# Optimization experiments

Measured on AMD Instinct MI355X. Metric: run time of the kernel, lower is better.

The kernel has to match this reference:

```python
import jax, jax.numpy as jnp
import numpy as np

HID = 256

def _linear(x, W, b):
    # torch nn.Linear: x @ W.T + b
    return x @ W.T + b

def setup_inputs() -> dict:
    key = jax.random.key(0)
    ks = jax.random.split(key, 9)
    N = 8192
    s = 1.0 / np.sqrt(HID)
    inp = {
        'query': jax.random.normal(ks[0], (N, HID), dtype=jnp.float32),
        'key':   jax.random.normal(ks[1], (N, HID), dtype=jnp.float32),
        'value': jax.random.normal(ks[2], (N, HID), dtype=jnp.float32),
        'Wq': jax.random.uniform(ks[3], (HID, HID), jnp.float32, -s, s),
        'bq': jax.random.uniform(ks[4], (HID,), jnp.float32, -s, s),
        'Wk': jax.random.uniform(ks[5], (HID, HID), jnp.float32, -s, s),
        'bk': jax.random.uniform(ks[6], (HID,), jnp.float32, -s, s),
        'Wv': jax.random.uniform(ks[7], (HID, HID), jnp.float32, -s, s),
        'bv': jax.random.uniform(ks[8], (HID,), jnp.float32, -s, s),
    }
    return inp

def reference(query, key, value, Wq, bq, Wk, bk, Wv, bv):
    q = _linear(query, Wq, bq)            # [N, H]
    k = _linear(key, Wk, bk)              # [N, H]
    v = _linear(value, Wv, bv)            # [N, H]
    q = q.reshape(-1, HID)
    k = k.reshape(-1, HID)
    v = v.reshape(-1, HID)
    attn = jax.nn.sigmoid(q @ k.T)        # [N, N], sigmoid attention (no softmax)
    return attn @ v                       # [N, H]
```

## Files before the change

### kernel.cpp

```cpp
#include <hip/hip_runtime.h>
#include <hip/hip_bf16.h>
#include <stdint.h>

#define HID 256
#define NTOK 8192

typedef unsigned short u16;
typedef unsigned int u32;

typedef __bf16 bf16x8 __attribute__((ext_vector_type(8)));
typedef float f32x4 __attribute__((ext_vector_type(4)));

__device__ __forceinline__ u16 f2bf(float f) {
  u32 u = __float_as_uint(f);
  u32 r = (u + 0x7FFFu + ((u >> 16) & 1u)) >> 16;
  return (u16)r;
}

__device__ __forceinline__ int swz(int row, int col, int ld) {
  return row * ld + ((((col >> 3) ^ (row & 7)) << 3) | (col & 7));
}

__global__ __launch_bounds__(256, 2) void proj_kernel(
    const float* __restrict__ Xq, const float* __restrict__ Xk, const float* __restrict__ Xv,
    const float* __restrict__ Wq, const float* __restrict__ Bq,
    const float* __restrict__ Wk, const float* __restrict__ Bk,
    const float* __restrict__ Wv, const float* __restrict__ Bv,
    u16* __restrict__ oq, u16* __restrict__ ok, u16* __restrict__ ovt)
{
  __shared__ __attribute__((aligned(16))) u16 Xs[64 * 64];
  __shared__ __attribute__((aligned(16))) u16 Ws[256 * 64];
  __shared__ __attribute__((aligned(16))) u16 Ts[64 * 256];

  const int tid = threadIdx.x;
  const int bid = blockIdx.x;
  const int sel = bid >> 7;
  const int m0 = (bid & 127) << 6;

  const float* X = sel == 0 ? Xq : (sel == 1 ? Xk : Xv);
  const float* W = sel == 0 ? Wq : (sel == 1 ? Wk : Wv);
  const float* B = sel == 0 ? Bq : (sel == 1 ? Bk : Bv);

  const int wid = tid >> 6;
  const int lane = tid & 63;
  const int ln = lane & 15;
  const int hi = lane >> 4;
  const int trow = tid >> 2;
  const int tq = tid & 3;

  f32x4 acc[4][4];
#pragma unroll
  for (int i = 0; i < 4; ++i)
#pragma unroll
    for (int j = 0; j < 4; ++j) acc[i][j] = (f32x4)0.f;

  for (int kc = 0; kc < 4; ++kc) {
    const int k0 = kc << 6;
    {
      const float* g = X + (size_t)(m0 + trow) * HID + k0 + tq * 16;
      u16 tmp[16];
#pragma unroll
      for (int e = 0; e < 16; e += 4) {
        float4 v = *reinterpret_cast<const float4*>(g + e);
        tmp[e] = f2bf(v.x); tmp[e + 1] = f2bf(v.y);
        tmp[e + 2] = f2bf(v.z); tmp[e + 3] = f2bf(v.w);
      }
      *reinterpret_cast<uint4*>(&Xs[swz(trow, tq * 16, 64)]) = *reinterpret_cast<uint4*>(&tmp[0]);
      *reinterpret_cast<uint4*>(&Xs[swz(trow, tq * 16 + 8, 64)]) = *reinterpret_cast<uint4*>(&tmp[8]);
    }
#pragma unroll
    for (int p = 0; p < 4; ++p) {
      int n = p * 64 + trow;
      const float* g = W + (size_t)n * HID + k0 + tq * 16;
      u16 tmp[16];
#pragma unroll
      for (int e = 0; e < 16; e += 4) {
        float4 v = *reinterpret_cast<const float4*>(g + e);
        tmp[e] = f2bf(v.x); tmp[e + 1] = f2bf(v.y);
        tmp[e + 2] = f2bf(v.z); tmp[e + 3] = f2bf(v.w);
      }
      *reinterpret_cast<uint4*>(&Ws[swz(n, tq * 16, 64)]) = *reinterpret_cast<uint4*>(&tmp[0]);
      *reinterpret_cast<uint4*>(&Ws[swz(n, tq * 16 + 8, 64)]) = *reinterpret_cast<uint4*>(&tmp[8]);
    }
    __syncthreads();
#pragma unroll
    for (int kk = 0; kk < 64; kk += 32) {
      bf16x8 a[4], b[4];
#pragma unroll
      for (int i = 0; i < 4; ++i)
        a[i] = *reinterpret_cast<bf16x8*>(&Xs[swz(i * 16 + ln, kk + hi * 8, 64)]);
#pragma unroll
      for (int j = 0; j < 4; ++j)
        b[j] = *reinterpret_cast<bf16x8*>(&Ws[swz(wid * 64 + j * 16 + ln, kk + hi * 8, 64)]);
#pragma unroll
      for (int i = 0; i < 4; ++i)
#pragma unroll
        for (int j = 0; j < 4; ++j)
          acc[i][j] = __builtin_amdgcn_mfma_f32_16x16x32_bf16(a[i], b[j], acc[i][j], 0, 0, 0);
    }
    __syncthreads();
  }

#pragma unroll
  for (int j = 0; j < 4; ++j) {
    int col = wid * 64 + j * 16 + ln;
    float bv = B[col];
#pragma unroll
    for (int i = 0; i < 4; ++i)
#pragma unroll
      for (int r = 0; r < 4; ++r) {
        int row = i * 16 + hi * 4 + r;
        Ts[row * HID + col] = f2bf(acc[i][j][r] + bv);
      }
  }
  __syncthreads();

  if (sel < 2) {
    u16* o = sel == 0 ? oq : ok;
#pragma unroll
    for (int i = 0; i < 8; ++i) {
      int slot = i * 256 + tid;
      int row = slot >> 5, s = slot & 31;
      uint4 v = *reinterpret_cast<uint4*>(&Ts[row * HID + s * 8]);
      *reinterpret_cast<uint4*>(&o[(size_t)(m0 + row) * HID + s * 8]) = v;
    }
  } else {
#pragma unroll
    for (int p = 0; p < 4; ++p) {
      int n = p * 64 + trow;
      int mseg = tq * 16;
      u16 tmp[16];
#pragma unroll
      for (int j2 = 0; j2 < 16; ++j2)
        tmp[j2] = Ts[(mseg + j2) * HID + n];
      *reinterpret_cast<uint4*>(&ovt[(size_t)n * NTOK + m0 + mseg]) = *reinterpret_cast<uint4*>(&tmp[0]);
      *reinterpret_cast<uint4*>(&ovt[(size_t)n * NTOK + m0 + mseg + 8]) = *reinterpret_cast<uint4*>(&tmp[8]);
    }
  }
}

#define QB 128
#define KVB 64
#define NSLICE 4
#define SLICE_LEN (NTOK / NSLICE)
#define NCH (SLICE_LEN / KVB)

__global__ __launch_bounds__(512, 2) void attn_kernel(
    const u16* __restrict__ qw, const u16* __restrict__ kw,
    const u16* __restrict__ vtw, float* __restrict__ out)
{
  __shared__ __attribute__((aligned(16))) u16 Qs[QB * HID];
  __shared__ __attribute__((aligned(16))) u16 Ks[KVB * HID];
  __shared__ __attribute__((aligned(16))) u16 Vs[HID * KVB];
  __shared__ __attribute__((aligned(16))) u16 Ps[QB * KVB];

  const int tid = threadIdx.x;
  const int bid = blockIdx.x;
  const int qt = bid >> 2, slice = bid & 3;
  const int m0 = qt * QB;
  const int kvbase = slice * SLICE_LEN;

  const int wid = tid >> 6, lane = tid & 63;
  const int ln = lane & 15, hi = lane >> 4;
  const int wr = wid >> 1, wc = wid & 1;

  auto stageQ = [&]() {
    int r_in = lane >> 5, s = lane & 31;
    for (int i = wid; i < 64; i += 8) {
      int r = i * 2 + r_in;
      const u16* g = qw + (size_t)(m0 + r) * HID + ((s ^ (r & 7)) << 3);
      __builtin_amdgcn_global_load_lds((const __attribute__((address_space(1))) u32*)g,
                                       (__attribute__((address_space(3))) u32*)(&Qs[i * 512]),
                                       16, 0, 0);
    }
  };
  auto stageK = [&](int ch) {
    int j0 = kvbase + ch * KVB;
    int r_in = lane >> 5, s = lane & 31;
    for (int i = wid; i < 32; i += 8) {
      int r = i * 2 + r_in;
      const u16* g = kw + (size_t)(j0 + r) * HID + ((s ^ (r & 7)) << 3);
      __builtin_amdgcn_global_load_lds((const __attribute__((address_space(1))) u32*)g,
                                       (__attribute__((address_space(3))) u32*)(&Ks[i * 512]),
                                       16, 0, 0);
    }
  };
  auto stageV = [&](int ch) {
    int j0 = kvbase + ch * KVB;
    int r_in = lane >> 3, s = lane & 7;
    for (int i = wid; i < 32; i += 8) {
      int d = i * 8 + r_in;
      const u16* g = vtw + (size_t)d * NTOK + j0 + ((s ^ (d & 7)) << 3);
      __builtin_amdgcn_global_load_lds((const __attribute__((address_space(1))) u32*)g,
                                       (__attribute__((address_space(3))) u32*)(&Vs[i * 512]),
                                       16, 0, 0);
    }
  };

  stageQ();
  stageK(0);
  stageV(0);

  f32x4 oacc[2][8];
#pragma unroll
  for (int i = 0; i < 2; ++i)
#pragma unroll
    for (int cb = 0; cb < 8; ++cb) oacc[i][cb] = (f32x4)0.f;

  __syncthreads();

  for (int c = 0; c < NCH; ++c) {
    f32x4 sacc[2][2];
#pragma unroll
    for (int i = 0; i < 2; ++i)
#pragma unroll
      for (int j = 0; j < 2; ++j) sacc[i][j] = (f32x4)0.f;

#pragma unroll
    for (int kk = 0; kk < 8; ++kk) {
      bf16x8 aq[2], bk[2];
#pragma unroll
      for (int i = 0; i < 2; ++i) {
        int qr = wr * 32 + i * 16 + ln;
        aq[i] = *reinterpret_cast<bf16x8*>(&Qs[qr * HID + ((((kk * 4 + hi) ^ (qr & 7))) << 3)]);
      }
#pragma unroll
      for (int j = 0; j < 2; ++j) {
        int kr = wc * 32 + j * 16 + ln;
        bk[j] = *reinterpret_cast<bf16x8*>(&Ks[kr * HID + ((((kk * 4 + hi) ^ (kr & 7))) << 3)]);
      }
#pragma unroll
      for (int i = 0; i < 2; ++i)
#pragma unroll
        for (int j = 0; j < 2; ++j)
          sacc[i][j] = __builtin_amdgcn_mfma_f32_16x16x32_bf16(aq[i], bk[j], sacc[i][j], 0, 0, 0);
    }

#pragma unroll
    for (int i = 0; i < 2; ++i)
#pragma unroll
      for (int j = 0; j < 2; ++j)
#pragma unroll
        for (int r = 0; r < 4; ++r) {
          float s = sacc[i][j][r];
          float p = __builtin_amdgcn_rcpf(1.0f + __expf(-s));
          int prow = wr * 32 + i * 16 + hi * 4 + r;
          int pcol = wc * 32 + j * 16 + ln;
          Ps[swz(prow, pcol, KVB)] = f2bf(p);
        }

    __syncthreads();
    if (c + 1 < NCH) stageK(c + 1);

#pragma unroll
    for (int ks = 0; ks < 2; ++ks) {
      bf16x8 ap[2];
#pragma unroll
      for (int i = 0; i < 2; ++i) {
        int pr = wr * 32 + i * 16 + ln;
        ap[i] = *reinterpret_cast<bf16x8*>(&Ps[pr * KVB + ((((ks * 4 + hi) ^ (pr & 7))) << 3)]);
      }
#pragma unroll
      for (int cb = 0; cb < 8; ++cb) {
        int vr = wc * 128 + cb * 16 + ln;
        bf16x8 bv = *reinterpret_cast<bf16x8*>(&Vs[vr * KVB + ((((ks * 4 + hi) ^ (vr & 7))) << 3)]);
#pragma unroll
        for (int i = 0; i < 2; ++i)
          oacc[i][cb] = __builtin_amdgcn_mfma_f32_16x16x32_bf16(ap[i], bv, oacc[i][cb], 0, 0, 0);
      }
    }

    __syncthreads();
    if (c + 1 < NCH) stageV(c + 1);
  }

#pragma unroll
  for (int i = 0; i < 2; ++i)
#pragma unroll
    for (int cb = 0; cb < 8; ++cb)
#pragma unroll
      for (int r = 0; r < 4; ++r) {
        int row = m0 + wr * 32 + i * 16 + hi * 4 + r;
        int col = wc * 128 + cb * 16 + ln;
        atomicAdd(&out[(size_t)row * HID + col], oacc[i][cb][r]);
      }
}

extern "C" void kernel_launch(void* const* d_in, const int* in_sizes, int n_in,
                              void* d_out, int out_size, void* d_ws, size_t ws_size,
                              hipStream_t stream) {
  const float* query = (const float*)d_in[0];
  const float* key_  = (const float*)d_in[1];
  const float* value = (const float*)d_in[2];
  const float* Wq = (const float*)d_in[3];
  const float* bq = (const float*)d_in[4];
  const float* Wk = (const float*)d_in[5];
  const float* bk = (const float*)d_in[6];
  const float* Wv = (const float*)d_in[7];
  const float* bv = (const float*)d_in[8];
  float* out = (float*)d_out;

  u16* qws  = (u16*)d_ws;
  u16* kws  = qws + (size_t)NTOK * HID;
  u16* vtws = kws + (size_t)NTOK * HID;

  hipMemsetAsync(d_out, 0, (size_t)NTOK * HID * sizeof(float), stream);
  proj_kernel<<<384, 256, 0, stream>>>(query, key_, value, Wq, bq, Wk, bk, Wv, bv,
                                       qws, kws, vtws);
  attn_kernel<<<256, 512, 0, stream>>>(qws, kws, vtws, out);
}
```

Measured before the change: 205.9 us.

## Rewrite attention with register-resident Q, 32x32 MFMA, permlane P, split-K fp16 partials

Rewrites all kernels. The attention kernel now holds a 256-row Q tile in registers per block and uses 32x32x16 MFMAs. It double-buffers K/V chunks of 32 tokens and passes sigmoid probabilities between lanes with permlane32 swaps instead of going through LDS. The key range is split into 8 slices that write fp16 partials, and a separate reduce kernel sums them, replacing the memset and float atomics. Weight conversion is moved to its own prepass and the projection is retiled to 128 rows. The cost is extra kernel launches, partial-buffer traffic, and fp16 range/precision risk in the partial outputs.

```diff
diff --git a/kernel.cpp b/kernel.cpp
--- a/kernel.cpp
+++ b/kernel.cpp
@@ -4,286 +4,268 @@
 
 #define HID 256
 #define NTOK 8192
+#define NS 8
+#define SLICE (NTOK / NS)
+#define CHUNK 32
+#define NCH (SLICE / CHUNK)
 
 typedef unsigned short u16;
 typedef unsigned int u32;
-
 typedef __bf16 bf16x8 __attribute__((ext_vector_type(8)));
-typedef float f32x4 __attribute__((ext_vector_type(4)));
+typedef float f32x16 __attribute__((ext_vector_type(16)));
+typedef __fp16 h16x2 __attribute__((ext_vector_type(2)));
+
+#define TAU(r, h) (((r) & 3) + 8 * ((r) >> 2) + 4 * (h))
 
 __device__ __forceinline__ u16 f2bf(float f) {
   u32 u = __float_as_uint(f);
-  u32 r = (u + 0x7FFFu + ((u >> 16) & 1u)) >> 16;
-  return (u16)r;
-}
-
-__device__ __forceinline__ int swz(int row, int col, int ld) {
-  return row * ld + ((((col >> 3) ^ (row & 7)) << 3) | (col & 7));
+  return (u16)((u + 0x7FFFu + ((u >> 16) & 1u)) >> 16);
+}
+
+__device__ __forceinline__ u32 cvtpk_bf16(float a, float b) {
+  u32 r;
+  asm("v_cvt_pk_bf16_f32 %0, %1, %2" : "=v"(r) : "v"(a), "v"(b));
+  return r;
+}
+
+__global__ void wcvt_kernel(const float* __restrict__ Wq, const float* __restrict__ Wk,
+                            const float* __restrict__ Wv, u16* __restrict__ out) {
+  int idx = blockIdx.x * 256 + threadIdx.x;
+  int mat = idx >> 14;
+  int off = (idx & 16383) << 2;
+  const float* src = mat == 0 ? Wq : (mat == 1 ? Wk : Wv);
+  float4 v = *reinterpret_cast<const float4*>(src + off);
+  ushort4 o;
+  o.x = f2bf(v.x); o.y = f2bf(v.y); o.z = f2bf(v.z); o.w = f2bf(v.w);
+  *reinterpret_cast<ushort4*>(out + mat * 65536 + off) = o;
 }
 
 __global__ __launch_bounds__(256, 2) void proj_kernel(
     const float* __restrict__ Xq, const float* __restrict__ Xk, const float* __restrict__ Xv,
-    const float* __restrict__ Wq, const float* __restrict__ Bq,
-    const float* __restrict__ Wk, const float* __restrict__ Bk,
-    const float* __restrict__ Wv, const float* __restrict__ Bv,
+    const u16* __restrict__ wcvt,
+    const float* __restrict__ Bq, const float* __restrict__ Bk, const float* __restrict__ Bv,
     u16* __restrict__ oq, u16* __restrict__ ok, u16* __restrict__ ovt)
 {
-  __shared__ __attribute__((aligned(16))) u16 Xs[64 * 64];
-  __shared__ __attribute__((aligned(16))) u16 Ws[256 * 64];
-  __shared__ __attribute__((aligned(16))) u16 Ts[64 * 256];
-
-  const int tid = threadIdx.x;
-  const int bid = blockIdx.x;
-  const int sel = bid >> 7;
-  const int m0 = (bid & 127) << 6;
+  __shared__ __attribute__((aligned(16))) unsigned char smem[32768 + 4 * 4352];
+  u16* wbuf0 = (u16*)smem;
+  u16* wbuf1 = (u16*)(smem + 16384);
+  float* scratch = (float*)(smem + 32768 + (threadIdx.x >> 6) * 4352);
+
+  const int tid = threadIdx.x, bid = blockIdx.x;
+  const int sel = bid >> 6;
+  const int m0 = (bid & 63) << 7;
+  const int wid = tid >> 6, l = tid & 63;
+  const int l31 = l & 31, lh = l >> 5;
 
   const float* X = sel == 0 ? Xq : (sel == 1 ? Xk : Xv);
-  const float* W = sel == 0 ? Wq : (sel == 1 ? Wk : Wv);
+  const u16* W = wcvt + sel * 65536;
   const float* B = sel == 0 ? Bq : (sel == 1 ? Bk : Bv);
-
-  const int wid = tid >> 6;
-  const int lane = tid & 63;
-  const int ln = lane & 15;
-  const int hi = lane >> 4;
-  const int trow = tid >> 2;
-  const int tq = tid & 3;
-
-  f32x4 acc[4][4];
-#pragma unroll
-  for (int i = 0; i < 4; ++i)
-#pragma unroll
-    for (int j = 0; j < 4; ++j) acc[i][j] = (f32x4)0.f;
-
-  for (int kc = 0; kc < 4; ++kc) {
-    const int k0 = kc << 6;
-    {
-      const float* g = X + (size_t)(m0 + trow) * HID + k0 + tq * 16;
+  const int mrow = m0 + wid * 32 + l31;
+
+  f32x16 acc[8];
+#pragma unroll
+  for (int nt = 0; nt < 8; ++nt) acc[nt] = (f32x16)0.f;
+
+  auto stageW = [&](int kc, u16* buf) {
+#pragma unroll
+    for (int ii = 0; ii < 4; ++ii) {
+      int u = (wid * 4 + ii) * 64 + l;
+      int ol = u >> 8, n = u & 255;
+      const u16* g = W + n * HID + kc * 32 + ol * 8;
+      __builtin_amdgcn_global_load_lds((const __attribute__((address_space(1))) u32*)g,
+                                       (__attribute__((address_space(3))) u32*)(buf + (size_t)u * 8),
+                                       16, 0, 0);
+    }
+  };
+
+  stageW(0, wbuf0);
+  __syncthreads();
+  for (int kc = 0; kc < 8; ++kc) {
+    u16* cur = (kc & 1) ? wbuf1 : wbuf0;
+    if (kc < 7) stageW(kc + 1, (kc & 1) ? wbuf0 : wbuf1);
+#pragma unroll
+    for (int k2 = 0; k2 < 2; ++k2) {
+      int ks = kc * 2 + k2;
+      float4 a0 = *reinterpret_cast<const float4*>(X + (size_t)mrow * HID + ks * 16 + lh * 8);
+      float4 a1 = *reinterpret_cast<const float4*>(X + (size_t)mrow * HID + ks * 16 + lh * 8 + 4);
+      union { u16 u[8]; bf16x8 v; } au;
+      au.u[0] = f2bf(a0.x); au.u[1] = f2bf(a0.y); au.u[2] = f2bf(a0.z); au.u[3] = f2bf(a0.w);
+      au.u[4] = f2bf(a1.x); au.u[5] = f2bf(a1.y); au.u[6] = f2bf(a1.z); au.u[7] = f2bf(a1.w);
+#pragma unroll
+      for (int nt = 0; nt < 8; ++nt) {
+        int unit = (k2 * 2 + lh) * 256 + nt * 32 + l31;
+        bf16x8 b = *reinterpret_cast<bf16x8*>(cur + (size_t)unit * 8);
+        acc[nt] = __builtin_amdgcn_mfma_f32_32x32x16_bf16(au.v, b, acc[nt], 0, 0, 0);
+      }
+    }
+    __syncthreads();
+  }
+
+#pragma unroll
+  for (int nt = 0; nt < 8; ++nt) {
+    float bv = B[nt * 32 + l31];
+#pragma unroll
+    for (int r = 0; r < 16; ++r)
+      scratch[TAU(r, lh) * 33 + l31] = acc[nt][r] + bv;
+    if (sel < 2) {
+      u16* o = sel == 0 ? oq : ok;
       u16 tmp[16];
 #pragma unroll
-      for (int e = 0; e < 16; e += 4) {
-        float4 v = *reinterpret_cast<const float4*>(g + e);
-        tmp[e] = f2bf(v.x); tmp[e + 1] = f2bf(v.y);
-        tmp[e + 2] = f2bf(v.z); tmp[e + 3] = f2bf(v.w);
-      }
-      *reinterpret_cast<uint4*>(&Xs[swz(trow, tq * 16, 64)]) = *reinterpret_cast<uint4*>(&tmp[0]);
-      *reinterpret_cast<uint4*>(&Xs[swz(trow, tq * 16 + 8, 64)]) = *reinterpret_cast<uint4*>(&tmp[8]);
-    }
-#pragma unroll
-    for (int p = 0; p < 4; ++p) {
-      int n = p * 64 + trow;
-      const float* g = W + (size_t)n * HID + k0 + tq * 16;
+      for (int c = 0; c < 16; ++c) tmp[c] = f2bf(scratch[l31 * 33 + lh * 16 + c]);
+      u16* dst = o + (size_t)(m0 + wid * 32 + l31) * HID + nt * 32 + lh * 16;
+      *reinterpret_cast<uint4*>(dst) = *reinterpret_cast<uint4*>(&tmp[0]);
+      *reinterpret_cast<uint4*>(dst + 8) = *reinterpret_cast<uint4*>(&tmp[8]);
+    } else {
       u16 tmp[16];
 #pragma unroll
-      for (int e = 0; e < 16; e += 4) {
-        float4 v = *reinterpret_cast<const float4*>(g + e);
-        tmp[e] = f2bf(v.x); tmp[e + 1] = f2bf(v.y);
-        tmp[e + 2] = f2bf(v.z); tmp[e + 3] = f2bf(v.w);
-      }
-      *reinterpret_cast<uint4*>(&Ws[swz(n, tq * 16, 64)]) = *reinterpret_cast<uint4*>(&tmp[0]);
-      *reinterpret_cast<uint4*>(&Ws[swz(n, tq * 16 + 8, 64)]) = *reinterpret_cast<uint4*>(&tmp[8]);
-    }
-    __syncthreads();
-#pragma unroll
-    for (int kk = 0; kk < 64; kk += 32) {
-      bf16x8 a[4], b[4];
-#pragma unroll
-      for (int i = 0; i < 4; ++i)
-        a[i] = *reinterpret_cast<bf16x8*>(&Xs[swz(i * 16 + ln, kk + hi * 8, 64)]);
-#pragma unroll
-      for (int j = 0; j < 4; ++j)
-        b[j] = *reinterpret_cast<bf16x8*>(&Ws[swz(wid * 64 + j * 16 + ln, kk + hi * 8, 64)]);
-#pragma unroll
-      for (int i = 0; i < 4; ++i)
-#pragma unroll
-        for (int j = 0; j < 4; ++j)
-          acc[i][j] = __builtin_amdgcn_mfma_f32_16x16x32_bf16(a[i], b[j], acc[i][j], 0, 0, 0);
-    }
-    __syncthreads();
-  }
-
-#pragma unroll
-  for (int j = 0; j < 4; ++j) {
-    int col = wid * 64 + j * 16 + ln;
-    float bv = B[col];
-#pragma unroll
-    for (int i = 0; i < 4; ++i)
-#pragma unroll
-      for (int r = 0; r < 4; ++r) {
-        int row = i * 16 + hi * 4 + r;
-        Ts[row * HID + col] = f2bf(acc[i][j][r] + bv);
-      }
-  }
-  __syncthreads();
-
-  if (sel < 2) {
-    u16* o = sel == 0 ? oq : ok;
-#pragma unroll
-    for (int i = 0; i < 8; ++i) {
-      int slot = i * 256 + tid;
-      int row = slot >> 5, s = slot & 31;
-      uint4 v = *reinterpret_cast<uint4*>(&Ts[row * HID + s * 8]);
-      *reinterpret_cast<uint4*>(&o[(size_t)(m0 + row) * HID + s * 8]) = v;
-    }
-  } else {
-#pragma unroll
-    for (int p = 0; p < 4; ++p) {
-      int n = p * 64 + trow;
-      int mseg = tq * 16;
-      u16 tmp[16];
-#pragma unroll
-      for (int j2 = 0; j2 < 16; ++j2)
-        tmp[j2] = Ts[(mseg + j2) * HID + n];
-      *reinterpret_cast<uint4*>(&ovt[(size_t)n * NTOK + m0 + mseg]) = *reinterpret_cast<uint4*>(&tmp[0]);
-      *reinterpret_cast<uint4*>(&ovt[(size_t)n * NTOK + m0 + mseg + 8]) = *reinterpret_cast<uint4*>(&tmp[8]);
-    }
-  }
-}
-
-#define QB 128
-#define KVB 64
-#define NSLICE 4
-#define SLICE_LEN (NTOK / NSLICE)
-#define NCH (SLICE_LEN / KVB)
+      for (int c = 0; c < 16; ++c) tmp[c] = f2bf(scratch[(lh * 16 + c) * 33 + l31]);
+      u16* dst = ovt + (size_t)(nt * 32 + l31) * NTOK + m0 + wid * 32 + lh * 16;
+      *reinterpret_cast<uint4*>(dst) = *reinterpret_cast<uint4*>(&tmp[0]);
+      *reinterpret_cast<uint4*>(dst + 8) = *reinterpret_cast<uint4*>(&tmp[8]);
+    }
+  }
+}
 
 __global__ __launch_bounds__(512, 2) void attn_kernel(
     const u16* __restrict__ qw, const u16* __restrict__ kw,
-    const u16* __restrict__ vtw, float* __restrict__ out)
+    const u16* __restrict__ vtw, u16* __restrict__ partial)
 {
-  __shared__ __attribute__((aligned(16))) u16 Qs[QB * HID];
-  __shared__ __attribute__((aligned(16))) u16 Ks[KVB * HID];
-  __shared__ __attribute__((aligned(16))) u16 Vs[HID * KVB];
-  __shared__ __attribute__((aligned(16))) u16 Ps[QB * KVB];
-
-  const int tid = threadIdx.x;
-  const int bid = blockIdx.x;
-  const int qt = bid >> 2, slice = bid & 3;
-  const int m0 = qt * QB;
-  const int kvbase = slice * SLICE_LEN;
-
-  const int wid = tid >> 6, lane = tid & 63;
-  const int ln = lane & 15, hi = lane >> 4;
-  const int wr = wid >> 1, wc = wid & 1;
-
-  auto stageQ = [&]() {
-    int r_in = lane >> 5, s = lane & 31;
-    for (int i = wid; i < 64; i += 8) {
-      int r = i * 2 + r_in;
-      const u16* g = qw + (size_t)(m0 + r) * HID + ((s ^ (r & 7)) << 3);
+  __shared__ __attribute__((aligned(16))) unsigned char smem[65536];
+  u16* kb0 = (u16*)smem;            u16* kb1 = (u16*)(smem + 16384);
+  u16* vb0 = (u16*)(smem + 32768);  u16* vb1 = (u16*)(smem + 49152);
+
+  const int tid = threadIdx.x, bid = blockIdx.x;
+  const int slice = bid & 7, qt = bid >> 3;
+  const int q0 = qt * 256;
+  const int tokbase = slice * SLICE;
+  const int wq = tid >> 6, l = tid & 63;
+  const int l31 = l & 31, lh = l >> 5;
+  const int qrow = q0 + wq * 32 + l31;
+
+  bf16x8 qB[16];
+#pragma unroll
+  for (int ks = 0; ks < 16; ++ks)
+    qB[ks] = *reinterpret_cast<const bf16x8*>(qw + (size_t)qrow * HID + ks * 16 + lh * 8);
+
+  auto stageK = [&](int c, u16* buf) {
+    int tok0 = tokbase + c * CHUNK;
+#pragma unroll
+    for (int ii = 0; ii < 2; ++ii) {
+      int u = (wq * 2 + ii) * 64 + l;
+      int o = u >> 5, t = u & 31;
+      const u16* g = kw + (size_t)(tok0 + t) * HID + o * 8;
       __builtin_amdgcn_global_load_lds((const __attribute__((address_space(1))) u32*)g,
-                                       (__attribute__((address_space(3))) u32*)(&Qs[i * 512]),
+                                       (__attribute__((address_space(3))) u32*)(buf + (size_t)u * 8),
                                        16, 0, 0);
     }
   };
-  auto stageK = [&](int ch) {
-    int j0 = kvbase + ch * KVB;
-    int r_in = lane >> 5, s = lane & 31;
-    for (int i = wid; i < 32; i += 8) {
-      int r = i * 2 + r_in;
-      const u16* g = kw + (size_t)(j0 + r) * HID + ((s ^ (r & 7)) << 3);
+  auto stageV = [&](int c, u16* buf) {
+    int tok0 = tokbase + c * CHUNK;
+#pragma unroll
+    for (int ii = 0; ii < 2; ++ii) {
+      int u = (wq * 2 + ii) * 64 + l;
+      int j = u >> 8, d = u & 255;
+      const u16* g = vtw + (size_t)d * NTOK + tok0 + j * 8;
       __builtin_amdgcn_global_load_lds((const __attribute__((address_space(1))) u32*)g,
-                                       (__attribute__((address_space(3))) u32*)(&Ks[i * 512]),
+                                       (__attribute__((address_space(3))) u32*)(buf + (size_t)u * 8),
                                        16, 0, 0);
     }
   };
-  auto stageV = [&](int ch) {
-    int j0 = kvbase + ch * KVB;
-    int r_in = lane >> 3, s = lane & 7;
-    for (int i = wid; i < 32; i += 8) {
-      int d = i * 8 + r_in;
-      const u16* g = vtw + (size_t)d * NTOK + j0 + ((s ^ (d & 7)) << 3);
-      __builtin_amdgcn_global_load_lds((const __attribute__((address_space(1))) u32*)g,
-                                       (__attribute__((address_space(3))) u32*)(&Vs[i * 512]),
-                                       16, 0, 0);
-    }
-  };
-
-  stageQ();
-  stageK(0);
-  stageV(0);
-
-  f32x4 oacc[2][8];
-#pragma unroll
-  for (int i = 0; i < 2; ++i)
-#pragma unroll
-    for (int cb = 0; cb < 8; ++cb) oacc[i][cb] = (f32x4)0.f;
-
+
+  f32x16 oacc[8];
+#pragma unroll
+  for (int dt = 0; dt < 8; ++dt) oacc[dt] = (f32x16)0.f;
+
+  stageK(0, kb0);
+  stageV(0, vb0);
   __syncthreads();
 
   for (int c = 0; c < NCH; ++c) {
-    f32x4 sacc[2][2];
-#pragma unroll
-    for (int i = 0; i < 2; ++i)
-#pragma unroll
-      for (int j = 0; j < 2; ++j) sacc[i][j] = (f32x4)0.f;
-
-#pragma unroll
-    for (int kk = 0; kk < 8; ++kk) {
-      bf16x8 aq[2], bk[2];
-#pragma unroll
-      for (int i = 0; i < 2; ++i) {
-        int qr = wr * 32 + i * 16 + ln;
-        aq[i] = *reinterpret_cast<bf16x8*>(&Qs[qr * HID + ((((kk * 4 + hi) ^ (qr & 7))) << 3)]);
+    u16* kc_ = (c & 1) ? kb1 : kb0;
+    u16* vc_ = (c & 1) ? vb1 : vb0;
+    if (c + 1 < NCH) {
+      stageK(c + 1, (c & 1) ? kb0 : kb1);
+      stageV(c + 1, (c & 1) ? vb0 : vb1);
+    }
+
+    f32x16 sacc = (f32x16)0.f;
+#pragma unroll
+    for (int ks = 0; ks < 16; ++ks) {
+      bf16x8 kf = *reinterpret_cast<bf16x8*>(kc_ + (size_t)((ks * 2 + lh) * 32 + l31) * 8);
+      sacc = __builtin_amdgcn_mfma_f32_32x32x16_bf16(kf, qB[ks], sacc, 0, 0, 0);
+    }
+
+    float p[16];
+#pragma unroll
+    for (int r = 0; r < 16; ++r) {
+      float e = __expf(-sacc[r]);
+      p[r] = __builtin_amdgcn_rcpf(1.0f + e);
+    }
+
+    u32 w0[4], w1[4];
+    {
+      u32 x0 = cvtpk_bf16(p[0], p[1]),  y0 = cvtpk_bf16(p[4], p[5]);
+      asm volatile("v_permlane32_swap_b32 %0, %1" : "+v"(x0), "+v"(y0));
+      u32 x1 = cvtpk_bf16(p[2], p[3]),  y1 = cvtpk_bf16(p[6], p[7]);
+      asm volatile("v_permlane32_swap_b32 %0, %1" : "+v"(x1), "+v"(y1));
+      w0[0] = x0; w0[1] = x1; w0[2] = y0; w0[3] = y1;
+      u32 x2 = cvtpk_bf16(p[8], p[9]),  y2 = cvtpk_bf16(p[12], p[13]);
+      asm volatile("v_permlane32_swap_b32 %0, %1" : "+v"(x2), "+v"(y2));
+      u32 x3 = cvtpk_bf16(p[10], p[11]), y3 = cvtpk_bf16(p[14], p[15]);
+      asm volatile("v_permlane32_swap_b32 %0, %1" : "+v"(x3), "+v"(y3));
+      w1[0] = x2; w1[1] = x3; w1[2] = y2; w1[3] = y3;
+    }
+
+#pragma unroll
+    for (int kp = 0; kp < 2; ++kp) {
+      union { u32 u[4]; bf16x8 v; } pb;
+      pb.u[0] = kp ? w1[0] : w0[0]; pb.u[1] = kp ? w1[1] : w0[1];
+      pb.u[2] = kp ? w1[2] : w0[2]; pb.u[3] = kp ? w1[3] : w0[3];
+#pragma unroll
+      for (int dt = 0; dt < 8; ++dt) {
+        bf16x8 vf = *reinterpret_cast<bf16x8*>(vc_ + (size_t)((kp * 2 + lh) * 256 + dt * 32 + l31) * 8);
+        oacc[dt] = __builtin_amdgcn_mfma_f32_32x32x16_bf16(vf, pb.v, oacc[dt], 0, 0, 0);
       }
-#pragma unroll
-      for (int j = 0; j < 2; ++j) {
-        int kr = wc * 32 + j * 16 + ln;
-        bk[j] = *reinterpret_cast<bf16x8*>(&Ks[kr * HID + ((((kk * 4 + hi) ^ (kr & 7))) << 3)]);
-      }
-#pragma unroll
-      for (int i = 0; i < 2; ++i)
-#pragma unroll
-        for (int j = 0; j < 2; ++j)
-          sacc[i][j] = __builtin_amdgcn_mfma_f32_16x16x32_bf16(aq[i], bk[j], sacc[i][j], 0, 0, 0);
-    }
-
-#pragma unroll
-    for (int i = 0; i < 2; ++i)
-#pragma unroll
-      for (int j = 0; j < 2; ++j)
-#pragma unroll
-        for (int r = 0; r < 4; ++r) {
-          float s = sacc[i][j][r];
-          float p = __builtin_amdgcn_rcpf(1.0f + __expf(-s));
-          int prow = wr * 32 + i * 16 + hi * 4 + r;
-          int pcol = wc * 32 + j * 16 + ln;
-          Ps[swz(prow, pcol, KVB)] = f2bf(p);
-        }
+    }
 
     __syncthreads();
-    if (c + 1 < NCH) stageK(c + 1);
-
-#pragma unroll
-    for (int ks = 0; ks < 2; ++ks) {
-      bf16x8 ap[2];
-#pragma unroll
-      for (int i = 0; i < 2; ++i) {
-        int pr = wr * 32 + i * 16 + ln;
-        ap[i] = *reinterpret_cast<bf16x8*>(&Ps[pr * KVB + ((((ks * 4 + hi) ^ (pr & 7))) << 3)]);
-      }
-#pragma unroll
-      for (int cb = 0; cb < 8; ++cb) {
-        int vr = wc * 128 + cb * 16 + ln;
-        bf16x8 bv = *reinterpret_cast<bf16x8*>(&Vs[vr * KVB + ((((ks * 4 + hi) ^ (vr & 7))) << 3)]);
-#pragma unroll
-        for (int i = 0; i < 2; ++i)
-          oacc[i][cb] = __builtin_amdgcn_mfma_f32_16x16x32_bf16(ap[i], bv, oacc[i][cb], 0, 0, 0);
-      }
-    }
-
-    __syncthreads();
-    if (c + 1 < NCH) stageV(c + 1);
-  }
-
-#pragma unroll
-  for (int i = 0; i < 2; ++i)
-#pragma unroll
-    for (int cb = 0; cb < 8; ++cb)
-#pragma unroll
-      for (int r = 0; r < 4; ++r) {
-        int row = m0 + wr * 32 + i * 16 + hi * 4 + r;
-        int col = wc * 128 + cb * 16 + ln;
-        atomicAdd(&out[(size_t)row * HID + col], oacc[i][cb][r]);
-      }
+  }
+
+  float* scratch = (float*)(smem + wq * 4352);
+  u16* part = partial + (size_t)slice * NTOK * HID;
+#pragma unroll
+  for (int dt = 0; dt < 8; ++dt) {
+#pragma unroll
+    for (int r = 0; r < 16; ++r)
+      scratch[TAU(r, lh) * 33 + l31] = oacc[dt][r];
+    u32 pk[8];
+#pragma unroll
+    for (int c2 = 0; c2 < 8; ++c2) {
+      float f0 = scratch[(lh * 16 + 2 * c2) * 33 + l31];
+      float f1 = scratch[(lh * 16 + 2 * c2 + 1) * 33 + l31];
+      union { h16x2 h; u32 u; } cv;
+      cv.h = __builtin_amdgcn_cvt_pkrtz(f0, f1);
+      pk[c2] = cv.u;
+    }
+    u16* dst = part + (size_t)qrow * HID + dt * 32 + lh * 16;
+    *reinterpret_cast<uint4*>(dst) = *reinterpret_cast<uint4*>(&pk[0]);
+    *reinterpret_cast<uint4*>(dst + 8) = *reinterpret_cast<uint4*>(&pk[4]);
+  }
+}
+
+__global__ void reduce_kernel(const u16* __restrict__ partial, float* __restrict__ out) {
+  size_t idx = (size_t)blockIdx.x * 256 + threadIdx.x;
+  size_t base = idx * 8;
+  float a[8] = {0.f, 0.f, 0.f, 0.f, 0.f, 0.f, 0.f, 0.f};
+#pragma unroll
+  for (int s = 0; s < NS; ++s) {
+    uint4 v = *reinterpret_cast<const uint4*>(partial + (size_t)s * NTOK * HID + base);
+    const __fp16* h = (const __fp16*)&v;
+#pragma unroll
+    for (int e = 0; e < 8; ++e) a[e] += (float)h[e];
+  }
+  *reinterpret_cast<float4*>(out + base) = make_float4(a[0], a[1], a[2], a[3]);
+  *reinterpret_cast<float4*>(out + base + 4) = make_float4(a[4], a[5], a[6], a[7]);
 }
 
 extern "C" void kernel_launch(void* const* d_in, const int* in_sizes, int n_in,
@@ -300,12 +282,16 @@
   const float* bv = (const float*)d_in[8];
   float* out = (float*)d_out;
 
-  u16* qws  = (u16*)d_ws;
-  u16* kws  = qws + (size_t)NTOK * HID;
-  u16* vtws = kws + (size_t)NTOK * HID;
-
-  hipMemsetAsync(d_out, 0, (size_t)NTOK * HID * sizeof(float), stream);
-  proj_kernel<<<384, 256, 0, stream>>>(query, key_, value, Wq, bq, Wk, bk, Wv, bv,
+  unsigned char* ws = (unsigned char*)d_ws;
+  u16* qws  = (u16*)(ws);
+  u16* kws  = (u16*)(ws + (4u << 20));
+  u16* vtws = (u16*)(ws + (8u << 20));
+  u16* wcvt = (u16*)(ws + (12u << 20));
+  u16* part = (u16*)(ws + (13u << 20));
+
+  wcvt_kernel<<<192, 256, 0, stream>>>(Wq, Wk, Wv, wcvt);
+  proj_kernel<<<192, 256, 0, stream>>>(query, key_, value, wcvt, bq, bk, bv,
                                        qws, kws, vtws);
-  attn_kernel<<<256, 512, 0, stream>>>(qws, kws, vtws, out);
-}
+  attn_kernel<<<256, 512, 0, stream>>>(qws, kws, vtws, part);
+  reduce_kernel<<<1024, 256, 0, stream>>>(part, out);
+}
```

After: 184.7 us. -10.3%, faster.
